# Performance work log

Measured on AMD Instinct MI355X. Metric: run time of the kernel, lower is better.

The kernel has to match this reference:

```python
import jax, jax.numpy as jnp
import numpy as np

IMAGE_SIZE = 1024
DOWNSIZING = 64
THRESHOLD = 0.65  # default_threshold_target (threshold arg == 0)
NUM_BG_POINTS = 1
ORI_SHAPE = (2160, 3840)
EMBED_C, FEAT_H, FEAT_W = 256, 64, 64


def setup_inputs() -> dict:
    key = jax.random.key(0)
    k1, k2 = jax.random.split(key)
    image_embeddings = jax.random.normal(k1, (1, EMBED_C, FEAT_H, FEAT_W), dtype=jnp.float32)
    reference_feat = jax.random.normal(k2, (1, EMBED_C), dtype=jnp.float32) * 0.1
    ori_shape = jnp.array(ORI_SHAPE, dtype=jnp.int32)
    return {"image_embeddings": image_embeddings, "reference_feat": reference_feat, "ori_shape": ori_shape}


def _postprocess_masks(sim, H, W):
    # F.interpolate to (image_size, image_size), crop to pre-padded size, resize to ori_shape
    sim = jax.image.resize(sim, (1, 1, IMAGE_SIZE, IMAGE_SIZE), method="bilinear", antialias=False)
    scale = IMAGE_SIZE / max(H, W)
    ph = int(np.floor(H * scale + 0.5))
    pw = int(np.floor(W * scale + 0.5))
    sim = sim[..., :ph, :pw]
    return jax.image.resize(sim, (1, 1, H, W), method="bilinear", antialias=False)


def reference(image_embeddings, reference_feat, ori_shape):
    H, W = int(ori_shape[0]), int(ori_shape[1])
    # --- similarity map ---
    t = image_embeddings[0]                                   # (C, hf, wf)
    c, hf, wf = t.shape
    t = t / jnp.linalg.norm(t, axis=0, keepdims=True)         # channel-wise L2 norm
    sim = (reference_feat @ t.reshape(c, hf * wf)).reshape(1, 1, hf, wf)
    sim = _postprocess_masks(sim, H, W)
    m = sim[0, 0]                                             # (H, W)
    flat = m.reshape(-1)                                      # (H*W,)
    hw = H * W

    # --- background points: k smallest values ---
    _, bg_idx = jax.lax.top_k(-flat, NUM_BG_POINTS)
    bg_row = bg_idx // W
    bg_col = bg_idx % W
    bg_coords = jnp.stack([bg_col, bg_row], axis=1).astype(jnp.float32)  # (N, 2) = (x, y)

    # --- foreground points: grid-binned per-cell max (segment-max form of
    #     torch.where + unique + broadcast-equality + per-bin topk) ---
    ratio = IMAGE_SIZE / max(H, W)
    n_cells_side = IMAGE_SIZE // DOWNSIZING                    # 16; bounds grid rows/cols
    num_cells = n_cells_side * n_cells_side                    # 256 fixed
    idx = jnp.arange(hw, dtype=jnp.int32)
    ys = idx // W
    xs = idx % W
    gy = jnp.floor(ys * (ratio / DOWNSIZING)).astype(jnp.int32)
    gx = jnp.floor(xs * (ratio / DOWNSIZING)).astype(jnp.int32)
    seg = gy * n_cells_side + gx                               # grid id per pixel

    valid = flat > THRESHOLD
    masked = jnp.where(valid, flat, -jnp.inf)
    seg_max = jax.ops.segment_max(masked, seg, num_segments=num_cells)
    # first pixel achieving the cell max (matches torch.topk tie behavior)
    is_max = valid & (masked == seg_max[seg])
    cand = jnp.where(is_max, idx, hw)
    best = jax.ops.segment_min(cand, seg, num_segments=num_cells)
    cell_valid = best < hw
    bi = jnp.minimum(best, hw - 1)
    px = (bi % W).astype(jnp.float32)
    py = (bi // W).astype(jnp.float32)
    ps = flat[bi]
    points = jnp.stack([px, py, ps], axis=1)                   # (num_cells, 3) = (x, y, score)
    points = jnp.where(cell_valid[:, None], points, -1.0)      # mimic F.pad(value=-1) rows
    sort_key = jnp.where(cell_valid, ps, -jnp.inf)
    order = jnp.argsort(-sort_key)                             # score descending, invalid last
    points_scores = points[order]
    return points_scores, bg_coords
```

## Files before the change

kernel.cpp:

```cpp
#include <hip/hip_runtime.h>

#define W_OUT 3840
#define H_OUT 2160
#define IW 1024
#define IH 576
#define BAND 240
#define RPB 4
#define NBLK (H_OUT / RPB)
#define BPB (BAND / RPB)

__device__ __forceinline__ unsigned int enc_f32(float f) {
    unsigned int b = __float_as_uint(f);
    return b ^ (0x80000000u | (unsigned int)((int)b >> 31));
}

__device__ __forceinline__ void release_vmem() {
    asm volatile("s_waitcnt vmcnt(0)" ::: "memory");
}

__global__ __launch_bounds__(256) void sim_kernel(
    const float* __restrict__ emb, const float* __restrict__ ref,
    float* __restrict__ sim,
    unsigned int* __restrict__ bandCnt,
    unsigned int* __restrict__ doneCnt)
{
    if (blockIdx.x == 0) {
        const int t = threadIdx.x;
        if (t < 9)          bandCnt[t * 16] = 0u;
        else if (t == 9)    *doneCnt = 0u;
    }
    const int lane = threadIdx.x & 63;
    const int wave = threadIdx.x >> 6;
    const int p = blockIdx.x * 64 + lane;
    const int cbase = wave * 64;
    float dot = 0.f, ss = 0.f;
#pragma unroll 8
    for (int cc = 0; cc < 64; ++cc) {
        int c = cbase + cc;
        float a = emb[c * 4096 + p];
        dot = fmaf(ref[c], a, dot);
        ss  = fmaf(a, a, ss);
    }
    __shared__ float sdot[4][64];
    __shared__ float sss[4][64];
    sdot[wave][lane] = dot;
    sss[wave][lane]  = ss;
    __syncthreads();
    if (wave == 0) {
        float d = (sdot[0][lane] + sdot[1][lane]) + (sdot[2][lane] + sdot[3][lane]);
        float s = (sss[0][lane] + sss[1][lane]) + (sss[2][lane] + sss[3][lane]);
        sim[p] = d / sqrtf(s);
    }
}

__global__ __launch_bounds__(256) void scan_kernel(
    const float* __restrict__ sim,
    unsigned long long* __restrict__ cellPart,
    unsigned long long* __restrict__ bgPart,
    unsigned long long* __restrict__ bandTab,
    unsigned long long* __restrict__ bgBand,
    unsigned int* __restrict__ bandCnt,
    unsigned int* __restrict__ doneCnt,
    float* __restrict__ out)
{
    __shared__ float4 IC4[3][IW / 4];
    __shared__ unsigned long long wmin[4];
    __shared__ unsigned long long bred[16][17];
    __shared__ unsigned int lastFlag;
    __shared__ float sk[256];

    const float INV375 = (float)(1.0 / 3.75);
    const float INV16  = 0.0625f;

    const int blk = blockIdx.x;
    const int y0  = blk * RPB;
    const int tid = threadIdx.x;
    const int band = y0 / BAND;

    {
        float fy0  = ((float)y0 + 0.5f) * INV375 - 0.5f;
        int ai0 = (int)floorf(fy0);
        int amin = min(max(ai0, 0), IH - 1);

        for (int k = 0; k < 3; ++k) {
            int a = amin + k;
            float fa  = ((float)a + 0.5f) * INV16 - 0.5f;
            float faf = floorf(fa);
            float wa  = fa - faf;
            int si = (int)faf;
            int s1 = min(max(si + 1, 0), 63);
            int s0 = min(max(si,     0), 63);
            const float* row0 = sim + s0 * 64;
            const float* row1 = sim + s1 * 64;
            float* dst = (float*)&IC4[k][0];
            for (int b = tid; b < IW; b += 256) {
                float fb  = ((float)b + 0.5f) * INV16 - 0.5f;
                float fbf = floorf(fb);
                float wb  = fb - fbf;
                int ci = (int)fbf;
                int c1 = min(max(ci + 1, 0), 63);
                int c0 = min(max(ci,     0), 63);
                float v0 = row0[c0] * (1.f - wb) + row0[c1] * wb;
                float v1 = row1[c0] * (1.f - wb) + row1[c1] * wb;
                dst[b] = v0 * (1.f - wa) + v1 * wa;
            }
        }
    }
    __syncthreads();

    unsigned long long bestCell = 0ull;
    unsigned long long bestBg   = 0xFFFFFFFFFFFFFFFFull;
    const int x0 = tid * 15;

    int amin;
    {
        float fy0 = ((float)y0 + 0.5f) * INV375 - 0.5f;
        amin = min(max((int)floorf(fy0), 0), IH - 1);
    }

#define UPD(F, jj) {                                                        \
        unsigned long long top = ((unsigned long long)enc_f32(F)) << 32;    \
        unsigned int idx = idxBase + (jj);                                  \
        unsigned long long bgk = top | (unsigned long long)idx;             \
        unsigned long long ck  = top | (unsigned long long)(~idx);          \
        if (ck  > bestCell) bestCell = ck;                                  \
        if (bgk < bestBg)   bestBg   = bgk;                                 \
    }

#pragma unroll 1
    for (int jr = 0; jr < RPB; ++jr) {
        const int y = y0 + jr;
        float fy  = ((float)y + 0.5f) * INV375 - 0.5f;
        float fyf = floorf(fy);
        float wy  = fy - fyf;
        int ai = (int)fyf;
        int a1 = min(max(ai + 1, 0), IH - 1);
        int a0 = min(max(ai,     0), IH - 1);
        const int i0 = a0 - amin;
        const int i1 = a1 - amin;
        const float* I0 = (const float*)&IC4[i0][0];
        const float* I1 = (const float*)&IC4[i1][0];
        const unsigned int idxBase = (unsigned int)(y * W_OUT + x0);

        if (tid == 0 || tid == 255) {
#pragma unroll
            for (int j = 0; j < 15; ++j) {
                int x = x0 + j;
                float fx  = ((float)x + 0.5f) * INV375 - 0.5f;
                float fxf = floorf(fx);
                float wx  = fx - fxf;
                int bi = (int)fxf;
                int b1 = min(max(bi + 1, 0), IW - 1);
                int b0 = min(max(bi,     0), IW - 1);
                float v0 = I0[b0] * (1.f - wx) + I0[b1] * wx;
                float v1 = I1[b0] * (1.f - wx) + I1[b1] * wx;
                float F  = v0 * (1.f - wy) + v1 * wy;
                UPD(F, j)
            }
        } else {
            float4 A0 = IC4[i0][tid - 1], B0 = IC4[i0][tid], C0 = IC4[i0][tid + 1];
            float4 A1 = IC4[i1][tid - 1], B1 = IC4[i1][tid], C1 = IC4[i1][tid + 1];
            const float rr0[12] = {A0.x,A0.y,A0.z,A0.w, B0.x,B0.y,B0.z,B0.w, C0.x,C0.y,C0.z,C0.w};
            const float rr1[12] = {A1.x,A1.y,A1.z,A1.w, B1.x,B1.y,B1.z,B1.w, C1.x,C1.y,C1.z,C1.w};

#define PX(j, i0w) {                                                        \
            float fx  = ((float)(x0 + (j)) + 0.5f) * INV375 - 0.5f;         \
            float fxf = floorf(fx);                                         \
            float wx  = fx - fxf;                                           \
            float v0 = rr0[(i0w)] * (1.f - wx) + rr0[(i0w) + 1] * wx;       \
            float v1 = rr1[(i0w)] * (1.f - wx) + rr1[(i0w) + 1] * wx;       \
            float F  = v0 * (1.f - wy) + v1 * wy;                           \
            UPD(F, j)                                                       \
        }
            PX(0,3)  PX(1,3)  PX(2,4)  PX(3,4)  PX(4,4)
            PX(5,4)  PX(6,5)  PX(7,5)  PX(8,5)  PX(9,6)
            PX(10,6) PX(11,6) PX(12,6) PX(13,7) PX(14,7)
#undef PX
        }
    }
#undef UPD

#pragma unroll
    for (int m = 1; m <= 8; m <<= 1) {
        unsigned long long o = __shfl_xor(bestCell, m, 64);
        if (o > bestCell) bestCell = o;
    }
    if ((tid & 15) == 0)
        atomicExch(&cellPart[blk * 16 + (tid >> 4)], bestCell);

#pragma unroll
    for (int m = 1; m <= 32; m <<= 1) {
        unsigned long long o = __shfl_xor(bestBg, m, 64);
        if (o < bestBg) bestBg = o;
    }
    if ((tid & 63) == 0) wmin[tid >> 6] = bestBg;
    __syncthreads();
    if (tid == 0) {
        unsigned long long b0 = wmin[0] < wmin[1] ? wmin[0] : wmin[1];
        unsigned long long b1 = wmin[2] < wmin[3] ? wmin[2] : wmin[3];
        atomicExch(&bgPart[blk], b0 < b1 ? b0 : b1);
        release_vmem();
        unsigned int old = atomicAdd(&bandCnt[band * 16], 1u);
        lastFlag = (old == (unsigned int)(BPB - 1)) ? 1u : 0u;
    }
    __syncthreads();
    if (!lastFlag) return;

    {
        const int cx  = tid & 15;
        const int sub = tid >> 4;
        unsigned long long* src = cellPart + (band * BPB) * 16 + cx;
        unsigned long long mx = 0ull;
#pragma unroll
        for (int i = 0; i < 4; ++i) {
            int r = sub * 4 + i;
            if (r < BPB) {
                unsigned long long v = atomicMax(&src[r * 16], 0ull);
                if (v > mx) mx = v;
            }
        }
        bred[sub][cx] = mx;

        unsigned long long bm = (tid < BPB)
            ? atomicMin(&bgPart[band * BPB + tid], 0xFFFFFFFFFFFFFFFFull)
            : 0xFFFFFFFFFFFFFFFFull;
#pragma unroll
        for (int m = 1; m <= 32; m <<= 1) {
            unsigned long long o = __shfl_xor(bm, m, 64);
            if (o < bm) bm = o;
        }
        if ((tid & 63) == 0) wmin[tid >> 6] = bm;
    }
    __syncthreads();
    if (tid < 16) {
        unsigned long long mx = bred[0][tid];
#pragma unroll
        for (int s = 1; s < 16; ++s) {
            unsigned long long v = bred[s][tid];
            if (v > mx) mx = v;
        }
        atomicExch(&bandTab[band * 16 + tid], mx);
    }
    if (tid == 0) {
        unsigned long long b0 = wmin[0] < wmin[1] ? wmin[0] : wmin[1];
        unsigned long long b1 = wmin[2] < wmin[3] ? wmin[2] : wmin[3];
        atomicExch(&bgBand[band], b0 < b1 ? b0 : b1);
    }
    __syncthreads();
    if (tid == 0) {
        release_vmem();
        unsigned int old = atomicAdd(doneCnt, 1u);
        lastFlag = (old == 8u) ? 1u : 0u;
    }
    __syncthreads();
    if (!lastFlag) return;

    float px = -1.f, py = -1.f, ps = -1.f;
    float key = -__builtin_huge_valf();
    if (tid < 144) {
        unsigned long long best = atomicMax(&bandTab[tid], 0ull);
        if (best != 0ull) {
            unsigned int e = (unsigned int)(best >> 32);
            unsigned int b = (e & 0x80000000u) ? (e ^ 0x80000000u) : ~e;
            float v = __uint_as_float(b);
            if (v > 0.65f) {
                unsigned int idx = ~((unsigned int)(best & 0xFFFFFFFFull));
                px = (float)(idx % W_OUT);
                py = (float)(idx / W_OUT);
                ps = v;
                key = v;
            }
        }
    }

    sk[tid] = key;
    __syncthreads();
    int rank = 0;
    for (int j = 0; j < 256; ++j) {
        float kj = sk[j];
        if (kj > key || (kj == key && j < tid)) rank++;
    }
    out[rank * 3 + 0] = px;
    out[rank * 3 + 1] = py;
    out[rank * 3 + 2] = ps;

    if (tid < 16) {
        unsigned long long b = (tid < 9) ? atomicMin(&bgBand[tid], 0xFFFFFFFFFFFFFFFFull)
                                         : 0xFFFFFFFFFFFFFFFFull;
#pragma unroll
        for (int m = 1; m <= 8; m <<= 1) {
            unsigned long long o = __shfl_xor(b, m, 64);
            if (o < b) b = o;
        }
        if (tid == 0) {
            unsigned int idx = (unsigned int)(b & 0xFFFFFFFFull);
            out[256 * 3 + 0] = (float)(idx % W_OUT);
            out[256 * 3 + 1] = (float)(idx / W_OUT);
        }
    }
}

extern "C" void kernel_launch(void* const* d_in, const int* in_sizes, int n_in,
                              void* d_out, int out_size, void* d_ws, size_t ws_size,
                              hipStream_t stream) {
    (void)in_sizes; (void)n_in; (void)out_size; (void)ws_size;
    const float* emb = (const float*)d_in[0];
    const float* ref = (const float*)d_in[1];
    float* out = (float*)d_out;

    char* ws = (char*)d_ws;
    float*              sim      = (float*)ws;
    unsigned long long* cellPart = (unsigned long long*)(ws + 16384);
    unsigned long long* bgPart   = (unsigned long long*)(ws + 85504);
    unsigned long long* bandTab  = (unsigned long long*)(ws + 89824);
    unsigned long long* bgBand   = (unsigned long long*)(ws + 90976);
    unsigned int*       bandCnt  = (unsigned int*)(ws + 91136);
    unsigned int*       doneCnt  = (unsigned int*)(ws + 91712);

    sim_kernel<<<64, 256, 0, stream>>>(emb, ref, sim, bandCnt, doneCnt);
    scan_kernel<<<NBLK, 256, 0, stream>>>(sim, cellPart, bgPart, bandTab, bgBand,
                                          bandCnt, doneCnt, out);
}
```

Measured before the change: 87.82 us.

## Fuse similarity computation into scan kernel, recomputing needed sim rows per block

Removes the separate sim_kernel launch. Each scan block now computes the up to three low-res similarity rows it needs directly from the embeddings into shared memory, and the counter reset moves to a hipMemsetAsync. This drops a kernel launch and the global round-trip of the sim map. In exchange, many blocks redundantly compute the same 256-channel dot products, and each thread runs a serial 256-iteration loop before the scan can begin.

Measured after the change: 97.76 us. 11.3% more time.

```diff
diff --git a/kernel.cpp b/kernel.cpp
--- a/kernel.cpp
+++ b/kernel.cpp
@@ -18,43 +18,9 @@
     asm volatile("s_waitcnt vmcnt(0)" ::: "memory");
 }
 
-__global__ __launch_bounds__(256) void sim_kernel(
-    const float* __restrict__ emb, const float* __restrict__ ref,
-    float* __restrict__ sim,
-    unsigned int* __restrict__ bandCnt,
-    unsigned int* __restrict__ doneCnt)
-{
-    if (blockIdx.x == 0) {
-        const int t = threadIdx.x;
-        if (t < 9)          bandCnt[t * 16] = 0u;
-        else if (t == 9)    *doneCnt = 0u;
-    }
-    const int lane = threadIdx.x & 63;
-    const int wave = threadIdx.x >> 6;
-    const int p = blockIdx.x * 64 + lane;
-    const int cbase = wave * 64;
-    float dot = 0.f, ss = 0.f;
-#pragma unroll 8
-    for (int cc = 0; cc < 64; ++cc) {
-        int c = cbase + cc;
-        float a = emb[c * 4096 + p];
-        dot = fmaf(ref[c], a, dot);
-        ss  = fmaf(a, a, ss);
-    }
-    __shared__ float sdot[4][64];
-    __shared__ float sss[4][64];
-    sdot[wave][lane] = dot;
-    sss[wave][lane]  = ss;
-    __syncthreads();
-    if (wave == 0) {
-        float d = (sdot[0][lane] + sdot[1][lane]) + (sdot[2][lane] + sdot[3][lane]);
-        float s = (sss[0][lane] + sss[1][lane]) + (sss[2][lane] + sss[3][lane]);
-        sim[p] = d / sqrtf(s);
-    }
-}
-
-__global__ __launch_bounds__(256) void scan_kernel(
-    const float* __restrict__ sim,
+__global__ __launch_bounds__(256) void fused_kernel(
+    const float* __restrict__ emb,
+    const float* __restrict__ ref,
     unsigned long long* __restrict__ cellPart,
     unsigned long long* __restrict__ bgPart,
     unsigned long long* __restrict__ bandTab,
@@ -63,6 +29,7 @@
     unsigned int* __restrict__ doneCnt,
     float* __restrict__ out)
 {
+    __shared__ float SIM3[3][64];
     __shared__ float4 IC4[3][IW / 4];
     __shared__ unsigned long long wmin[4];
     __shared__ unsigned long long bred[16][17];
@@ -77,33 +44,58 @@
     const int tid = threadIdx.x;
     const int band = y0 / BAND;
 
+    int amin, S;
     {
-        float fy0  = ((float)y0 + 0.5f) * INV375 - 0.5f;
-        int ai0 = (int)floorf(fy0);
-        int amin = min(max(ai0, 0), IH - 1);
-
-        for (int k = 0; k < 3; ++k) {
-            int a = amin + k;
-            float fa  = ((float)a + 0.5f) * INV16 - 0.5f;
-            float faf = floorf(fa);
-            float wa  = fa - faf;
-            int si = (int)faf;
-            int s1 = min(max(si + 1, 0), 63);
-            int s0 = min(max(si,     0), 63);
-            const float* row0 = sim + s0 * 64;
-            const float* row1 = sim + s1 * 64;
-            float* dst = (float*)&IC4[k][0];
-            for (int b = tid; b < IW; b += 256) {
-                float fb  = ((float)b + 0.5f) * INV16 - 0.5f;
-                float fbf = floorf(fb);
-                float wb  = fb - fbf;
-                int ci = (int)fbf;
-                int c1 = min(max(ci + 1, 0), 63);
-                int c0 = min(max(ci,     0), 63);
-                float v0 = row0[c0] * (1.f - wb) + row0[c1] * wb;
-                float v1 = row1[c0] * (1.f - wb) + row1[c1] * wb;
-                dst[b] = v0 * (1.f - wa) + v1 * wa;
+        float fy0 = ((float)y0 + 0.5f) * INV375 - 0.5f;
+        amin = min(max((int)floorf(fy0), 0), IH - 1);
+        float fa0 = ((float)amin + 0.5f) * INV16 - 0.5f;
+        S = min(max((int)floorf(fa0), 0), 63);
+    }
+
+    if (tid < 192) {
+        const int k   = tid >> 6;
+        const int col = tid & 63;
+        const int p   = min(S + k, 63) * 64 + col;
+        float dw[4], sw[4];
+#pragma unroll
+        for (int w = 0; w < 4; ++w) {
+            float dot = 0.f, ss = 0.f;
+#pragma unroll 8
+            for (int cc = 0; cc < 64; ++cc) {
+                int c = w * 64 + cc;
+                float a = emb[c * 4096 + p];
+                dot = fmaf(ref[c], a, dot);
+                ss  = fmaf(a, a, ss);
             }
+            dw[w] = dot; sw[w] = ss;
+        }
+        float d = (dw[0] + dw[1]) + (dw[2] + dw[3]);
+        float s = (sw[0] + sw[1]) + (sw[2] + sw[3]);
+        SIM3[k][col] = d / sqrtf(s);
+    }
+    __syncthreads();
+
+    for (int k = 0; k < 3; ++k) {
+        int a = amin + k;
+        float fa  = ((float)a + 0.5f) * INV16 - 0.5f;
+        float faf = floorf(fa);
+        float wa  = fa - faf;
+        int si = (int)faf;
+        int s1 = min(max(si + 1, 0), 63);
+        int s0 = min(max(si,     0), 63);
+        const float* row0 = &SIM3[s0 - S][0];
+        const float* row1 = &SIM3[s1 - S][0];
+        float* dst = (float*)&IC4[k][0];
+        for (int b = tid; b < IW; b += 256) {
+            float fb  = ((float)b + 0.5f) * INV16 - 0.5f;
+            float fbf = floorf(fb);
+            float wb  = fb - fbf;
+            int ci = (int)fbf;
+            int c1 = min(max(ci + 1, 0), 63);
+            int c0 = min(max(ci,     0), 63);
+            float v0 = row0[c0] * (1.f - wb) + row0[c1] * wb;
+            float v1 = row1[c0] * (1.f - wb) + row1[c1] * wb;
+            dst[b] = v0 * (1.f - wa) + v1 * wa;
         }
     }
     __syncthreads();
@@ -111,12 +103,6 @@
     unsigned long long bestCell = 0ull;
     unsigned long long bestBg   = 0xFFFFFFFFFFFFFFFFull;
     const int x0 = tid * 15;
-
-    int amin;
-    {
-        float fy0 = ((float)y0 + 0.5f) * INV375 - 0.5f;
-        amin = min(max((int)floorf(fy0), 0), IH - 1);
-    }
 
 #define UPD(F, jj) {                                                        \
         unsigned long long top = ((unsigned long long)enc_f32(F)) << 32;    \
@@ -309,15 +295,14 @@
     float* out = (float*)d_out;
 
     char* ws = (char*)d_ws;
-    float*              sim      = (float*)ws;
-    unsigned long long* cellPart = (unsigned long long*)(ws + 16384);
-    unsigned long long* bgPart   = (unsigned long long*)(ws + 85504);
-    unsigned long long* bandTab  = (unsigned long long*)(ws + 89824);
-    unsigned long long* bgBand   = (unsigned long long*)(ws + 90976);
-    unsigned int*       bandCnt  = (unsigned int*)(ws + 91136);
-    unsigned int*       doneCnt  = (unsigned int*)(ws + 91712);
-
-    sim_kernel<<<64, 256, 0, stream>>>(emb, ref, sim, bandCnt, doneCnt);
-    scan_kernel<<<NBLK, 256, 0, stream>>>(sim, cellPart, bgPart, bandTab, bgBand,
-                                          bandCnt, doneCnt, out);
+    unsigned long long* cellPart = (unsigned long long*)(ws + 0);
+    unsigned long long* bgPart   = (unsigned long long*)(ws + 69120);
+    unsigned long long* bandTab  = (unsigned long long*)(ws + 73440);
+    unsigned long long* bgBand   = (unsigned long long*)(ws + 74592);
+    unsigned int*       bandCnt  = (unsigned int*)(ws + 74688);
+    unsigned int*       doneCnt  = (unsigned int*)(ws + 75264);
+
+    hipMemsetAsync(ws + 74688, 0, 640, stream);
+    fused_kernel<<<NBLK, 256, 0, stream>>>(emb, ref, cellPart, bgPart, bandTab,
+                                           bgBand, bandCnt, doneCnt, out);
 }
```
